# Performance work log

Hardware: AMD Instinct MI355X
Metric: run time of the kernel (lower is better)

Reference implementation:

```python
import math
import jax
import jax.numpy as jnp
import numpy as np

B, T, D = 1, 2048, 1024
H, KV, DH = 16, 4, 64
E, TOPK, DFF = 32, 4, 1024
WINDOW = 128
EPS = 1e-5
ROPE_BASE = 150000.0
ROPE_SCALE = 32.0


def setup_inputs() -> dict:
    key = jax.random.key(0)
    ks = jax.random.split(key, 12)
    s = 0.02  # init scale for stability
    return {
        "x": jax.random.normal(ks[0], (B, T, D), jnp.float32),
        "attn_norm_w": 1.0 + 0.02 * jax.random.normal(ks[1], (D,), jnp.float32),
        "ffn_norm_w": 1.0 + 0.02 * jax.random.normal(ks[2], (D,), jnp.float32),
        "qkv_w": s * jax.random.normal(ks[3], (D, H * DH + 2 * KV * DH), jnp.float32),
        "qkv_b": s * jax.random.normal(ks[4], (H * DH + 2 * KV * DH,), jnp.float32),
        "proj_w": s * jax.random.normal(ks[5], (H * DH, D), jnp.float32),
        "proj_b": s * jax.random.normal(ks[6], (D,), jnp.float32),
        "attn_sink": 0.5 * jax.random.normal(ks[7], (H,), jnp.float32),
        "gate_w": s * jax.random.normal(ks[8], (D, E), jnp.float32),
        "gate_b": s * jax.random.normal(ks[9], (E,), jnp.float32),
        "W_up": s * jax.random.normal(ks[10], (E, D, 2 * DFF), jnp.float32),
        "W_down": s * jax.random.normal(ks[11], (E, DFF, D), jnp.float32),
    }


def _rmsnorm(x, w):
    rms = jax.lax.rsqrt(jnp.mean(x * x, axis=-1, keepdims=True) + EPS)
    return w * (x * rms)


def _apply_rope(x, sin, cos):
    # x: [B, h, T, dh]; sin/cos: [T, dh//2] -> interleaved rotation
    x1, x2 = x[..., ::2], x[..., 1::2]
    out = jnp.stack([x1 * cos - x2 * sin, x1 * sin + x2 * cos], axis=-1)
    return out.reshape(x.shape)


def reference(x, attn_norm_w, ffn_norm_w, qkv_w, qkv_b, proj_w, proj_b,
              attn_sink, gate_w, gate_b, W_up, W_down):
    Bx, Tx, Dx = x.shape
    # ---- attention branch ----
    h = _rmsnorm(x, attn_norm_w)
    qkv = h @ qkv_w + qkv_b
    q = qkv[..., : H * DH].reshape(Bx, Tx, H, DH).transpose(0, 2, 1, 3)
    k = qkv[..., H * DH : H * DH + KV * DH].reshape(Bx, Tx, KV, DH).transpose(0, 2, 1, 3)
    v = qkv[..., H * DH + KV * DH :].reshape(Bx, Tx, KV, DH).transpose(0, 2, 1, 3)
    # RoPE angles: pos/scale * base^{-2i/dh}
    pos = jnp.arange(Tx, dtype=jnp.float32) / ROPE_SCALE
    inv_freq = 1.0 / (ROPE_BASE ** (jnp.arange(0, DH, 2, dtype=jnp.float32) / DH))
    freqs = pos[:, None] * inv_freq[None, :]  # [T, DH//2]
    sin, cos = jnp.sin(freqs), jnp.cos(freqs)
    q = _apply_rope(q, sin, cos)
    k = _apply_rope(k, sin, cos)
    rep = H // KV
    k = jnp.repeat(k, rep, axis=1)
    v = jnp.repeat(v, rep, axis=1)
    logits = jnp.einsum('bhqd,bhkd->bhqk', q, k) / math.sqrt(DH)
    i = jnp.arange(Tx)[:, None]
    j = jnp.arange(Tx)[None, :]
    mask = (j > i) | (i - j > WINDOW)  # sliding-window causal
    logits = jnp.where(mask, -jnp.inf, logits)
    lse = jax.nn.logsumexp(logits, axis=-1, keepdims=True)  # [B,H,T,1]
    denom_log = jnp.logaddexp(lse, attn_sink.reshape(1, H, 1, 1))
    attn = jnp.exp(logits - denom_log)  # rows sum to < 1 due to sink
    y = jnp.einsum('bhqk,bhkd->bhqd', attn, v)
    y = y.transpose(0, 2, 1, 3).reshape(Bx, Tx, H * DH)
    x = x + (y @ proj_w + proj_b)
    # ---- token-choice MoE branch ----
    h2 = _rmsnorm(x, ffn_norm_w).reshape(Bx * Tx, Dx)
    glogits = h2 @ gate_w + gate_b  # [N, E]
    topv, topi = jax.lax.top_k(glogits, TOPK)
    gw = jax.nn.softmax(topv, axis=-1)  # [N, TOPK]
    N = Bx * Tx
    combine = jnp.zeros((N, E), x.dtype).at[jnp.arange(N)[:, None], topi].add(gw)
    def body(acc, we):
        wu, wd, ce = we  # [D,2DFF], [DFF,D], [N]
        ug = h2 @ wu
        u, g = ug[:, :DFF], ug[:, DFF:]
        return acc + ce[:, None] * ((jax.nn.silu(g) * u) @ wd), None
    y2, _ = jax.lax.scan(body, jnp.zeros_like(h2), (W_up, W_down, combine.T))
    return x + y2.reshape(Bx, Tx, Dx)
```

## Files before the change

### kernel.cpp

```cpp
#include <hip/hip_runtime.h>
#include <hip/hip_bf16.h>

#define NEx 32
#define QKVN 1536
#define MAXTILES 96

typedef __attribute__((ext_vector_type(4))) float f32x4_t;
typedef __attribute__((ext_vector_type(8))) __bf16 bf16x8_t;

__device__ __forceinline__ unsigned short f2bfu(float f) {
  union { float f; unsigned int u; } a; a.f = f;
  unsigned int r = a.u + 0x7fffu + ((a.u >> 16) & 1u);
  return (unsigned short)(r >> 16);
}
__device__ __forceinline__ float bf2f(unsigned short u) {
  union { unsigned int u; float f; } a; a.u = ((unsigned int)u) << 16; return a.f;
}
__device__ __forceinline__ uint2 pack4u(unsigned short a, unsigned short b,
                                        unsigned short c, unsigned short d) {
  return make_uint2((unsigned int)a | ((unsigned int)b << 16),
                    (unsigned int)c | ((unsigned int)d << 16));
}
__device__ __forceinline__ void split2(float v, unsigned short& hi, unsigned short& lo) {
  hi = f2bfu(v);
  lo = f2bfu(v - bf2f(hi));
}
typedef const __attribute__((address_space(1))) void* gas_t;
typedef __attribute__((address_space(3))) void* las_t;
__device__ __forceinline__ void gl16(const void* g, void* l) {
  __builtin_amdgcn_global_load_lds((gas_t)g, (las_t)l, 16, 0, 0);
}

template<int SPLIT>
__global__ __launch_bounds__(256) void k_wT(const float* __restrict__ in,
    unsigned short* __restrict__ outh, unsigned short* __restrict__ outl, int N) {
  __shared__ float T[64][68];
  int k0 = blockIdx.x * 64, n0 = blockIdx.y * 64, e = blockIdx.z;
  const float* src = in + (size_t)e * 1024 * N;
  int t = threadIdx.x;
  int rk = t >> 2, c4 = (t & 3) * 4;
#pragma unroll
  for (int j = 0; j < 4; ++j) {
    int col = c4 + j * 16;
    f32x4_t v = *(const f32x4_t*)(src + (size_t)(k0 + rk) * N + n0 + col);
    *(f32x4_t*)&T[rk][col] = v;
  }
  __syncthreads();
  int nn = t >> 2, kc0 = (t & 3) * 16;
  size_t orow = ((size_t)e * N + n0 + nn) * 1024 + k0;
#pragma unroll
  for (int j = 0; j < 2; ++j) {
    int kc = kc0 + j * 8;
    unsigned short hi[8], lo[8];
#pragma unroll
    for (int q = 0; q < 8; ++q) split2(T[kc + q][nn], hi[q], lo[q]);
    uint2 a = pack4u(hi[0], hi[1], hi[2], hi[3]);
    uint2 b = pack4u(hi[4], hi[5], hi[6], hi[7]);
    *(uint4*)(outh + orow + kc) = make_uint4(a.x, a.y, b.x, b.y);
    if (SPLIT) {
      uint2 c = pack4u(lo[0], lo[1], lo[2], lo[3]);
      uint2 d = pack4u(lo[4], lo[5], lo[6], lo[7]);
      *(uint4*)(outl + orow + kc) = make_uint4(c.x, c.y, d.x, d.y);
    }
  }
}

__global__ __launch_bounds__(256) void k_rmsnorm_s(const float* __restrict__ x,
    const float* __restrict__ w, unsigned short* __restrict__ ph, unsigned short* __restrict__ pl) {
  int row = blockIdx.x, tid = threadIdx.x;
  f32x4_t v = *(const f32x4_t*)(x + (size_t)row * 1024 + tid * 4);
  float ss = v.x * v.x + v.y * v.y + v.z * v.z + v.w * v.w;
#pragma unroll
  for (int o = 32; o > 0; o >>= 1) ss += __shfl_xor(ss, o);
  __shared__ float red[4];
  if ((tid & 63) == 0) red[tid >> 6] = ss;
  __syncthreads();
  float sc = rsqrtf((red[0] + red[1] + red[2] + red[3]) * (1.f / 1024.f) + 1e-5f);
  const float* wr = w + tid * 4;
  ushort4 h4, l4;
  split2(v.x * sc * wr[0], h4.x, l4.x);
  split2(v.y * sc * wr[1], h4.y, l4.y);
  split2(v.z * sc * wr[2], h4.z, l4.z);
  split2(v.w * sc * wr[3], h4.w, l4.w);
  *(ushort4*)(ph + (size_t)row * 1024 + tid * 4) = h4;
  *(ushort4*)(pl + (size_t)row * 1024 + tid * 4) = l4;
}

__global__ __launch_bounds__(256) void k_rmsnorm_f(const float* __restrict__ x,
    const float* __restrict__ w, float* __restrict__ outf, unsigned short* __restrict__ outb,
    float* __restrict__ y2) {
  int row = blockIdx.x, tid = threadIdx.x;
  f32x4_t v = *(const f32x4_t*)(x + (size_t)row * 1024 + tid * 4);
  *(f32x4_t*)(y2 + (size_t)row * 1024 + tid * 4) = (f32x4_t){0.f, 0.f, 0.f, 0.f};
  float ss = v.x * v.x + v.y * v.y + v.z * v.z + v.w * v.w;
#pragma unroll
  for (int o = 32; o > 0; o >>= 1) ss += __shfl_xor(ss, o);
  __shared__ float red[4];
  if ((tid & 63) == 0) red[tid >> 6] = ss;
  __syncthreads();
  float sc = rsqrtf((red[0] + red[1] + red[2] + red[3]) * (1.f / 1024.f) + 1e-5f);
  const float* wr = w + tid * 4;
  f32x4_t o4;
  o4.x = v.x * sc * wr[0]; o4.y = v.y * sc * wr[1];
  o4.z = v.z * sc * wr[2]; o4.w = v.w * sc * wr[3];
  *(f32x4_t*)(outf + (size_t)row * 1024 + tid * 4) = o4;
  ushort4 b4;
  b4.x = f2bfu(o4.x); b4.y = f2bfu(o4.y); b4.z = f2bfu(o4.z); b4.w = f2bfu(o4.w);
  *(ushort4*)(outb + (size_t)row * 1024 + tid * 4) = b4;
}

template<int RES>
__global__ __launch_bounds__(256) void k_gemm_s(
    const unsigned short* __restrict__ Ahg, const unsigned short* __restrict__ Alg,
    const unsigned short* __restrict__ BhT, const unsigned short* __restrict__ BlT,
    const float* __restrict__ bias, const float* __restrict__ res,
    float* __restrict__ C, int N) {
  __shared__ unsigned short Ah[64 * 32], Al[64 * 32], Bh[128 * 32], Bl[128 * 32];
  int tid = threadIdx.x, lane = tid & 63, w = tid >> 6;
  int m0 = blockIdx.y * 64, n0 = blockIdx.x * 128;
  int wm = (w >> 1) * 32, wn = (w & 1) * 64;
  int rl = lane >> 2, koff = (lane & 3) * 8;
  const unsigned short* agh = Ahg + (size_t)(m0 + w * 16 + rl) * 1024 + koff;
  const unsigned short* agl = Alg + (size_t)(m0 + w * 16 + rl) * 1024 + koff;
  const unsigned short* bgh0 = BhT + (size_t)(n0 + (w * 2 + 0) * 16 + rl) * 1024 + koff;
  const unsigned short* bgh1 = BhT + (size_t)(n0 + (w * 2 + 1) * 16 + rl) * 1024 + koff;
  const unsigned short* bgl0 = BlT + (size_t)(n0 + (w * 2 + 0) * 16 + rl) * 1024 + koff;
  const unsigned short* bgl1 = BlT + (size_t)(n0 + (w * 2 + 1) * 16 + rl) * 1024 + koff;
  f32x4_t acc[2][4];
#pragma unroll
  for (int i = 0; i < 2; ++i)
#pragma unroll
    for (int j = 0; j < 4; ++j) acc[i][j] = (f32x4_t){0.f, 0.f, 0.f, 0.f};
  int fr = lane & 15, fc = (lane >> 4) * 8;
  for (int k0 = 0; k0 < 1024; k0 += 32) {
    gl16(agh + k0, (char*)Ah + w * 1024);
    gl16(agl + k0, (char*)Al + w * 1024);
    gl16(bgh0 + k0, (char*)Bh + (w * 2 + 0) * 1024);
    gl16(bgh1 + k0, (char*)Bh + (w * 2 + 1) * 1024);
    gl16(bgl0 + k0, (char*)Bl + (w * 2 + 0) * 1024);
    gl16(bgl1 + k0, (char*)Bl + (w * 2 + 1) * 1024);
    __syncthreads();
    bf16x8_t fah[2], fal[2], fbh[4], fbl[4];
#pragma unroll
    for (int mi = 0; mi < 2; ++mi) {
      fah[mi] = *(const bf16x8_t*)(Ah + (wm + mi * 16 + fr) * 32 + fc);
      fal[mi] = *(const bf16x8_t*)(Al + (wm + mi * 16 + fr) * 32 + fc);
    }
#pragma unroll
    for (int nj = 0; nj < 4; ++nj) {
      fbh[nj] = *(const bf16x8_t*)(Bh + (wn + nj * 16 + fr) * 32 + fc);
      fbl[nj] = *(const bf16x8_t*)(Bl + (wn + nj * 16 + fr) * 32 + fc);
    }
#pragma unroll
    for (int mi = 0; mi < 2; ++mi)
#pragma unroll
      for (int nj = 0; nj < 4; ++nj) {
        acc[mi][nj] = __builtin_amdgcn_mfma_f32_16x16x32_bf16(fah[mi], fbh[nj], acc[mi][nj], 0, 0, 0);
        acc[mi][nj] = __builtin_amdgcn_mfma_f32_16x16x32_bf16(fah[mi], fbl[nj], acc[mi][nj], 0, 0, 0);
        acc[mi][nj] = __builtin_amdgcn_mfma_f32_16x16x32_bf16(fal[mi], fbh[nj], acc[mi][nj], 0, 0, 0);
      }
    __syncthreads();
  }
  int frow = (lane >> 4) * 4;
#pragma unroll
  for (int mi = 0; mi < 2; ++mi)
#pragma unroll
    for (int nj = 0; nj < 4; ++nj) {
      int col = n0 + wn + nj * 16 + fr;
      float bv = bias[col];
#pragma unroll
      for (int r = 0; r < 4; ++r) {
        int row = m0 + wm + mi * 16 + frow + r;
        float v = acc[mi][nj][r] + bv;
        if (RES) v += res[(size_t)row * N + col];
        C[(size_t)row * N + col] = v;
      }
    }
}

__global__ __launch_bounds__(256) void k_rope(float* __restrict__ qkv) {
  int idx = blockIdx.x * 256 + threadIdx.x;
  int i = idx & 31;
  int r5 = idx >> 5;
  int hd = r5 % 20, t = r5 / 20;
  int col = (hd < 16) ? hd * 64 : 1024 + (hd - 16) * 64;
  float* p = qkv + (size_t)t * QKVN + col + 2 * i;
  float2 v = *(float2*)p;
  float invf = exp2f(-(float)i * (17.194602975157967f / 32.f));
  float ang = ((float)t * (1.f / 32.f)) * invf;
  float s, c;
  sincosf(ang, &s, &c);
  float2 o; o.x = v.x * c - v.y * s; o.y = v.x * s + v.y * c;
  *(float2*)p = o;
}

__global__ __launch_bounds__(256) void k_attn(const float* __restrict__ qkv,
    const float* __restrict__ sink, unsigned short* __restrict__ yh,
    unsigned short* __restrict__ yl) {
  __shared__ float Kl[72 * 65];
  __shared__ float Vl[72 * 64];
  __shared__ float ql[16][64];
  __shared__ float pl[4][128];
  int i0 = blockIdx.x * 16, hh = blockIdx.y;
  int g = hh >> 2;
  int jb = i0 - 128; if (jb < 0) jb = 0;
  int nk = i0 + 16 - jb;
  int tid = threadIdx.x, wid = tid >> 6, lane = tid & 63;
  {
    int r = tid >> 4, d4 = (tid & 15) * 4;
    *(f32x4_t*)&ql[r][d4] = *(const f32x4_t*)(qkv + (size_t)(i0 + r) * QKVN + hh * 64 + d4);
  }
  float sk = sink[hh];
  float m_[4], s_[4], y_[4];
#pragma unroll
  for (int qq = 0; qq < 4; ++qq) { m_[qq] = sk; s_[qq] = 0.f; y_[qq] = 0.f; }
  int nch = (nk + 71) / 72;
  int cbase = 0;
  for (int ch = 0; ch < nch; ++ch) {
    int csz = nk - cbase; if (csz > 72) csz = 72;
    __syncthreads();
    for (int id = tid; id < csz * 16; id += 256) {
      int c = id >> 4, d4 = (id & 15) * 4;
      const float* kp = qkv + (size_t)(jb + cbase + c) * QKVN + 1024 + g * 64 + d4;
      *(f32x4_t*)&Kl[c * 65 + d4] = *(const f32x4_t*)kp;
      *(f32x4_t*)&Vl[c * 64 + d4] = *(const f32x4_t*)(kp + 256);
    }
    __syncthreads();
#pragma unroll
    for (int qq = 0; qq < 4; ++qq) {
      int qr = wid * 4 + qq;
      int cm = i0 + qr - jb;
      int s1 = lane + 64;
      int r1 = (s1 < csz) ? s1 : (csz - 1);
      const float* k0p = Kl + lane * 65;
      const float* k1p = Kl + r1 * 65;
      float a0 = 0.f, a1 = 0.f;
#pragma unroll 4
      for (int d = 0; d < 64; ++d) {
        float qd = ql[qr][d];
        a0 += qd * k0p[d];
        a1 += qd * k1p[d];
      }
      int c0 = cbase + lane, c1 = cbase + s1;
      bool ok0 = (lane < csz) && (c0 <= cm) && (c0 >= cm - 128);
      bool ok1 = (s1 < csz) && (c1 <= cm) && (c1 >= cm - 128);
      float l0 = ok0 ? a0 * 0.125f : -1e30f;
      float l1 = ok1 ? a1 * 0.125f : -1e30f;
      float mc = fmaxf(l0, l1);
#pragma unroll
      for (int o = 32; o > 0; o >>= 1) mc = fmaxf(mc, __shfl_xor(mc, o));
      float mo = m_[qq];
      float mn = fmaxf(mo, mc);
      float fac = __expf(mo - mn);
      float p0 = __expf(l0 - mn), p1 = __expf(l1 - mn);
      float ps = p0 + p1;
#pragma unroll
      for (int o = 32; o > 0; o >>= 1) ps += __shfl_xor(ps, o);
      m_[qq] = mn;
      s_[qq] = s_[qq] * fac + ps;
      pl[wid][lane] = p0;
      pl[wid][s1] = p1;
      __syncthreads();
      float y = y_[qq] * fac;
      for (int s = 0; s < csz; ++s) y += pl[wid][s] * Vl[s * 64 + lane];
      y_[qq] = y;
      __syncthreads();
    }
    cbase += csz;
  }
#pragma unroll
  for (int qq = 0; qq < 4; ++qq) {
    float inv = 1.f / (s_[qq] + __expf(sk - m_[qq]));
    int i = i0 + wid * 4 + qq;
    unsigned short hi, lo;
    split2(y_[qq] * inv, hi, lo);
    yh[(size_t)i * 1024 + hh * 64 + lane] = hi;
    yl[(size_t)i * 1024 + hh * 64 + lane] = lo;
  }
}

__global__ __launch_bounds__(64) void k_gate(const float* __restrict__ h2f,
    const float* __restrict__ gw, const float* __restrict__ gb,
    int* __restrict__ texp, float* __restrict__ twt) {
  int t = blockIdx.x, l = threadIdx.x;
  int e = l & 31, half = l >> 5;
  const float* hr = h2f + (size_t)t * 1024 + half * 512;
  const float* wp = gw + (size_t)half * 512 * 32 + e;
  float s = 0;
  for (int d = 0; d < 512; ++d) s += hr[d] * wp[(size_t)d * 32];
  s += __shfl_xor(s, 32);
  __shared__ float gl[32];
  if (l < 32) gl[l] = s + gb[e];
  __syncthreads();
  if (l == 0) {
    int bi[4]; float bv[4];
    for (int j = 0; j < 4; ++j) {
      int mi_ = 0; float mv = gl[0];
      for (int q = 1; q < 32; ++q) if (gl[q] > mv) { mv = gl[q]; mi_ = q; }
      bi[j] = mi_; bv[j] = mv; gl[mi_] = -1e30f;
    }
    float mx = bv[0], sum = 0, wv[4];
    for (int j = 0; j < 4; ++j) { wv[j] = __expf(bv[j] - mx); sum += wv[j]; }
    float inv = 1.f / sum;
    for (int j = 0; j < 4; ++j) { texp[t * 4 + j] = bi[j]; twt[t * 4 + j] = wv[j] * inv; }
  }
}

__global__ __launch_bounds__(256) void k_moe_count(const int* __restrict__ texp, int* __restrict__ cnt) {
  int e = blockIdx.x, tid = threadIdx.x;
  int c = 0;
  for (int i = tid; i < 8192; i += 256) c += (texp[i] == e);
#pragma unroll
  for (int o = 32; o > 0; o >>= 1) c += __shfl_xor(c, o);
  __shared__ int red[4];
  if ((tid & 63) == 0) red[tid >> 6] = c;
  __syncthreads();
  if (tid == 0) cnt[e] = red[0] + red[1] + red[2] + red[3];
}

__global__ void k_moe_off(const int* __restrict__ cnt, int* __restrict__ off,
                          int* __restrict__ tiles) {
  if (threadIdx.x == 0) {
    int s = 0, t = 0;
    for (int e = 0; e < NEx; ++e) {
      off[e] = s;
      int nt = (cnt[e] + 127) >> 7;
      for (int j = 0; j < nt; ++j) tiles[t++] = e | (j << 8);
      s += cnt[e];
    }
    for (; t < MAXTILES; ++t) tiles[t] = -1;
  }
}

__global__ __launch_bounds__(256) void k_moe_assign(const int* __restrict__ texp,
    const float* __restrict__ twt, const int* __restrict__ off,
    int* __restrict__ slot_token, float* __restrict__ slot_wt) {
  int e = blockIdx.x, tid = threadIdx.x;
  int b0 = tid * 32;
  int c = 0;
  for (int i = 0; i < 32; ++i) c += (texp[b0 + i] == e);
  __shared__ int pre[256];
  pre[tid] = c;
  __syncthreads();
  for (int d = 1; d < 256; d <<= 1) {
    int v = (tid >= d) ? pre[tid - d] : 0;
    __syncthreads();
    pre[tid] += v;
    __syncthreads();
  }
  int run = off[e] + pre[tid] - c;
  for (int i = 0; i < 32; ++i) {
    int idx = b0 + i;
    if (texp[idx] == e) {
      slot_token[run] = idx >> 2;
      slot_wt[run] = twt[idx];
      ++run;
    }
  }
}

__global__ __launch_bounds__(256) void k_moe_up(const unsigned short* __restrict__ h2b,
    const unsigned short* __restrict__ WupT, const int* __restrict__ cnt,
    const int* __restrict__ off, const int* __restrict__ tiles,
    const int* __restrict__ slot_token, unsigned short* __restrict__ act) {
  int code = tiles[blockIdx.y];
  if (code < 0) return;
  int e = code & 255;
  int m0 = (code >> 8) << 7;
  int ne = cnt[e];
  int n0 = blockIdx.x * 64;
  int base = off[e];
  __shared__ unsigned short Asm[128 * 32];
  __shared__ unsigned short Bsm[128 * 32];
  int tid = threadIdx.x, lane = tid & 63, w = tid >> 6;
  int rl = lane >> 2, koff = (lane & 3) * 8;
  const unsigned short* ag[2];
  const unsigned short* bg[2];
#pragma unroll
  for (int i = 0; i < 2; ++i) {
    int row = (w * 2 + i) * 16 + rl;
    int tok = (m0 + row < ne) ? slot_token[base + m0 + row] : 0;
    ag[i] = h2b + (size_t)tok * 1024 + koff;
    int grow = (row < 64) ? (n0 + row) : (1024 + n0 + row - 64);
    bg[i] = WupT + (size_t)e * 2048 * 1024 + (size_t)grow * 1024 + koff;
  }
  f32x4_t acc[2][8];
#pragma unroll
  for (int i = 0; i < 2; ++i)
#pragma unroll
    for (int j = 0; j < 8; ++j) acc[i][j] = (f32x4_t){0.f, 0.f, 0.f, 0.f};
  int fr = lane & 15, fc = (lane >> 4) * 8;
  for (int k0 = 0; k0 < 1024; k0 += 32) {
    gl16(ag[0] + k0, (char*)Asm + (w * 2 + 0) * 1024);
    gl16(ag[1] + k0, (char*)Asm + (w * 2 + 1) * 1024);
    gl16(bg[0] + k0, (char*)Bsm + (w * 2 + 0) * 1024);
    gl16(bg[1] + k0, (char*)Bsm + (w * 2 + 1) * 1024);
    __syncthreads();
    bf16x8_t af[2], bfr[8];
#pragma unroll
    for (int mi = 0; mi < 2; ++mi)
      af[mi] = *(const bf16x8_t*)(Asm + (w * 32 + mi * 16 + fr) * 32 + fc);
#pragma unroll
    for (int nj = 0; nj < 8; ++nj)
      bfr[nj] = *(const bf16x8_t*)(Bsm + (nj * 16 + fr) * 32 + fc);
#pragma unroll
    for (int mi = 0; mi < 2; ++mi)
#pragma unroll
      for (int nj = 0; nj < 8; ++nj)
        acc[mi][nj] = __builtin_amdgcn_mfma_f32_16x16x32_bf16(af[mi], bfr[nj], acc[mi][nj], 0, 0, 0);
    __syncthreads();
  }
  int frow = (lane >> 4) * 4;
#pragma unroll
  for (int mi = 0; mi < 2; ++mi)
#pragma unroll
    for (int r = 0; r < 4; ++r) {
      int row = m0 + w * 32 + mi * 16 + frow + r;
      if (row < ne) {
#pragma unroll
        for (int nj = 0; nj < 4; ++nj) {
          float u = acc[mi][nj][r];
          float gg = acc[mi][nj + 4][r];
          float sig = 1.f / (1.f + __expf(-gg));
          act[(size_t)(base + row) * 1024 + n0 + nj * 16 + fr] = f2bfu(u * gg * sig);
        }
      }
    }
}

__global__ __launch_bounds__(256) void k_moe_down(const unsigned short* __restrict__ act,
    const unsigned short* __restrict__ WdnT, const int* __restrict__ cnt,
    const int* __restrict__ off, const int* __restrict__ tiles,
    const int* __restrict__ slot_token, const float* __restrict__ slot_wt,
    float* __restrict__ y2) {
  int code = tiles[blockIdx.y];
  if (code < 0) return;
  int e = code & 255;
  int m0 = (code >> 8) << 7;
  int ne = cnt[e];
  int n0 = blockIdx.x * 128;
  int base = off[e];
  __shared__ unsigned short Asm[128 * 32];
  __shared__ unsigned short Bsm[128 * 32];
  int tid = threadIdx.x, lane = tid & 63, w = tid >> 6;
  int wm = (w >> 1) * 64, wn = (w & 1) * 64;
  int rl = lane >> 2, koff = (lane & 3) * 8;
  const unsigned short* ag[2];
  const unsigned short* bg[2];
#pragma unroll
  for (int i = 0; i < 2; ++i) {
    int row = (w * 2 + i) * 16 + rl;
    ag[i] = act + (size_t)(base + m0 + row) * 1024 + koff;
    bg[i] = WdnT + (size_t)e * 1024 * 1024 + (size_t)(n0 + row) * 1024 + koff;
  }
  f32x4_t acc[4][4];
#pragma unroll
  for (int i = 0; i < 4; ++i)
#pragma unroll
    for (int j = 0; j < 4; ++j) acc[i][j] = (f32x4_t){0.f, 0.f, 0.f, 0.f};
  int fr = lane & 15, fc = (lane >> 4) * 8;
  for (int k0 = 0; k0 < 1024; k0 += 32) {
    gl16(ag[0] + k0, (char*)Asm + (w * 2 + 0) * 1024);
    gl16(ag[1] + k0, (char*)Asm + (w * 2 + 1) * 1024);
    gl16(bg[0] + k0, (char*)Bsm + (w * 2 + 0) * 1024);
    gl16(bg[1] + k0, (char*)Bsm + (w * 2 + 1) * 1024);
    __syncthreads();
    bf16x8_t af[4], bfr[4];
#pragma unroll
    for (int mi = 0; mi < 4; ++mi)
      af[mi] = *(const bf16x8_t*)(Asm + (wm + mi * 16 + fr) * 32 + fc);
#pragma unroll
    for (int nj = 0; nj < 4; ++nj)
      bfr[nj] = *(const bf16x8_t*)(Bsm + (wn + nj * 16 + fr) * 32 + fc);
#pragma unroll
    for (int mi = 0; mi < 4; ++mi)
#pragma unroll
      for (int nj = 0; nj < 4; ++nj)
        acc[mi][nj] = __builtin_amdgcn_mfma_f32_16x16x32_bf16(af[mi], bfr[nj], acc[mi][nj], 0, 0, 0);
    __syncthreads();
  }
  int frow = (lane >> 4) * 4;
#pragma unroll
  for (int mi = 0; mi < 4; ++mi)
#pragma unroll
    for (int r = 0; r < 4; ++r) {
      int row = m0 + wm + mi * 16 + frow + r;
      if (row < ne) {
        int slot = base + row;
        int token = slot_token[slot];
        float wt = slot_wt[slot];
#pragma unroll
        for (int nj = 0; nj < 4; ++nj) {
          int col = n0 + wn + nj * 16 + fr;
          atomicAdd(&y2[(size_t)token * 1024 + col], wt * acc[mi][nj][r]);
        }
      }
    }
}

__global__ __launch_bounds__(256) void k_final(const float* __restrict__ x1,
    const float* __restrict__ y2, float* __restrict__ out) {
  int idx = blockIdx.x * 256 + threadIdx.x;
  f32x4_t a = *(const f32x4_t*)(x1 + (size_t)idx * 4);
  f32x4_t b = *(const f32x4_t*)(y2 + (size_t)idx * 4);
  a = a + b;
  *(f32x4_t*)(out + (size_t)idx * 4) = a;
}

extern "C" void kernel_launch(void* const* d_in, const int* in_sizes, int n_in,
                              void* d_out, int out_size, void* d_ws, size_t ws_size,
                              hipStream_t stream) {
  const float* x           = (const float*)d_in[0];
  const float* attn_norm_w = (const float*)d_in[1];
  const float* ffn_norm_w  = (const float*)d_in[2];
  const float* qkv_w       = (const float*)d_in[3];
  const float* qkv_b       = (const float*)d_in[4];
  const float* proj_w      = (const float*)d_in[5];
  const float* proj_b      = (const float*)d_in[6];
  const float* attn_sink   = (const float*)d_in[7];
  const float* gate_w      = (const float*)d_in[8];
  const float* gate_b      = (const float*)d_in[9];
  const float* W_up        = (const float*)d_in[10];
  const float* W_down      = (const float*)d_in[11];
  float* out = (float*)d_out;

  char* ws = (char*)d_ws;
  size_t o = 0;
  auto alloc = [&](size_t bytes) -> void* {
    void* p = ws + o;
    o = (o + bytes + 255) & ~(size_t)255;
    return p;
  };
  unsigned short* WT      = (unsigned short*)alloc((size_t)32 * 2048 * 1024 * 2);
  unsigned short* qkvThi  = (unsigned short*)alloc((size_t)1536 * 1024 * 2);
  unsigned short* qkvTlo  = (unsigned short*)alloc((size_t)1536 * 1024 * 2);
  unsigned short* projThi = (unsigned short*)alloc((size_t)1024 * 1024 * 2);
  unsigned short* projTlo = (unsigned short*)alloc((size_t)1024 * 1024 * 2);
  unsigned short* pAhi    = (unsigned short*)alloc((size_t)2048 * 1024 * 2);
  unsigned short* pAlo    = (unsigned short*)alloc((size_t)2048 * 1024 * 2);
  float* qkv              = (float*)alloc((size_t)2048 * 1536 * 4);
  float* x1               = (float*)alloc((size_t)2048 * 1024 * 4);
  unsigned short* act     = (unsigned short*)alloc((size_t)(8192 + 128) * 1024 * 2);
  float* y2               = (float*)alloc((size_t)2048 * 1024 * 4);
  int* texp               = (int*)alloc(8192 * 4);
  float* twt              = (float*)alloc(8192 * 4);
  int* cnt                = (int*)alloc(256);
  int* offs               = (int*)alloc(256);
  int* tiles              = (int*)alloc(MAXTILES * 4);
  int* slot_token         = (int*)alloc(8192 * 4);
  float* slot_wt          = (float*)alloc(8192 * 4);
  float* h2f              = qkv;
  unsigned short* h2b     = (unsigned short*)(qkv + (size_t)2048 * 1024);

  k_wT<1><<<dim3(16, 24, 1), 256, 0, stream>>>(qkv_w, qkvThi, qkvTlo, 1536);
  k_wT<1><<<dim3(16, 16, 1), 256, 0, stream>>>(proj_w, projThi, projTlo, 1024);
  k_wT<0><<<dim3(16, 32, 32), 256, 0, stream>>>(W_up, WT, nullptr, 2048);

  k_rmsnorm_s<<<2048, 256, 0, stream>>>(x, attn_norm_w, pAhi, pAlo);
  k_gemm_s<0><<<dim3(12, 32), 256, 0, stream>>>(pAhi, pAlo, qkvThi, qkvTlo, qkv_b, nullptr, qkv, 1536);
  k_rope<<<5120, 256, 0, stream>>>(qkv);
  k_attn<<<dim3(128, 16), 256, 0, stream>>>(qkv, attn_sink, pAhi, pAlo);
  k_gemm_s<1><<<dim3(8, 32), 256, 0, stream>>>(pAhi, pAlo, projThi, projTlo, proj_b, x, x1, 1024);
  k_rmsnorm_f<<<2048, 256, 0, stream>>>(x1, ffn_norm_w, h2f, h2b, y2);
  k_gate<<<2048, 64, 0, stream>>>(h2f, gate_w, gate_b, texp, twt);
  k_moe_count<<<32, 256, 0, stream>>>(texp, cnt);
  k_moe_off<<<1, 64, 0, stream>>>(cnt, offs, tiles);
  k_moe_assign<<<32, 256, 0, stream>>>(texp, twt, offs, slot_token, slot_wt);
  k_moe_up<<<dim3(16, MAXTILES), 256, 0, stream>>>(h2b, WT, cnt, offs, tiles, slot_token, act);
  k_wT<0><<<dim3(16, 16, 32), 256, 0, stream>>>(W_down, WT, nullptr, 1024);
  k_moe_down<<<dim3(8, MAXTILES), 256, 0, stream>>>(act, WT, cnt, offs, tiles, slot_token, slot_wt, y2);
  k_final<<<2048, 256, 0, stream>>>(x1, y2, out);
}
```

Before: 475.9 us.

## Restructure attention to batch four queries per warp and fuse residual into output

```diff
diff --git a/kernel.cpp b/kernel.cpp
--- a/kernel.cpp
+++ b/kernel.cpp
@@ -88,10 +88,10 @@
 
 __global__ __launch_bounds__(256) void k_rmsnorm_f(const float* __restrict__ x,
     const float* __restrict__ w, float* __restrict__ outf, unsigned short* __restrict__ outb,
-    float* __restrict__ y2) {
+    float* __restrict__ out) {
   int row = blockIdx.x, tid = threadIdx.x;
   f32x4_t v = *(const f32x4_t*)(x + (size_t)row * 1024 + tid * 4);
-  *(f32x4_t*)(y2 + (size_t)row * 1024 + tid * 4) = (f32x4_t){0.f, 0.f, 0.f, 0.f};
+  *(f32x4_t*)(out + (size_t)row * 1024 + tid * 4) = v;
   float ss = v.x * v.x + v.y * v.y + v.z * v.z + v.w * v.w;
 #pragma unroll
   for (int o = 32; o > 0; o >>= 1) ss += __shfl_xor(ss, o);
@@ -200,7 +200,7 @@
   __shared__ float Kl[72 * 65];
   __shared__ float Vl[72 * 64];
   __shared__ float ql[16][64];
-  __shared__ float pl[4][128];
+  __shared__ float pl[4][4][128];
   int i0 = blockIdx.x * 16, hh = blockIdx.y;
   int g = hh >> 2;
   int jb = i0 - 128; if (jb < 0) jb = 0;
@@ -216,6 +216,7 @@
   for (int qq = 0; qq < 4; ++qq) { m_[qq] = sk; s_[qq] = 0.f; y_[qq] = 0.f; }
   int nch = (nk + 71) / 72;
   int cbase = 0;
+  int qb = wid * 4;
   for (int ch = 0; ch < nch; ++ch) {
     int csz = nk - cbase; if (csz > 72) csz = 72;
     __syncthreads();
@@ -226,26 +227,30 @@
       *(f32x4_t*)&Vl[c * 64 + d4] = *(const f32x4_t*)(kp + 256);
     }
     __syncthreads();
+    int s1 = lane + 64;
+    int r1 = (s1 < csz) ? s1 : (csz - 1);
+    const float* k0p = Kl + lane * 65;
+    const float* k1p = Kl + r1 * 65;
+    float a0[4] = {0.f, 0.f, 0.f, 0.f}, a1[4] = {0.f, 0.f, 0.f, 0.f};
+#pragma unroll 4
+    for (int d = 0; d < 64; ++d) {
+      float k0 = k0p[d], k1 = k1p[d];
+#pragma unroll
+      for (int qq = 0; qq < 4; ++qq) {
+        float qd = ql[qb + qq][d];
+        a0[qq] += qd * k0;
+        a1[qq] += qd * k1;
+      }
+    }
+    int c0 = cbase + lane, c1 = cbase + s1;
+    float fac_[4];
 #pragma unroll
     for (int qq = 0; qq < 4; ++qq) {
-      int qr = wid * 4 + qq;
-      int cm = i0 + qr - jb;
-      int s1 = lane + 64;
-      int r1 = (s1 < csz) ? s1 : (csz - 1);
-      const float* k0p = Kl + lane * 65;
-      const float* k1p = Kl + r1 * 65;
-      float a0 = 0.f, a1 = 0.f;
-#pragma unroll 4
-      for (int d = 0; d < 64; ++d) {
-        float qd = ql[qr][d];
-        a0 += qd * k0p[d];
-        a1 += qd * k1p[d];
-      }
-      int c0 = cbase + lane, c1 = cbase + s1;
+      int cm = i0 + qb + qq - jb;
       bool ok0 = (lane < csz) && (c0 <= cm) && (c0 >= cm - 128);
       bool ok1 = (s1 < csz) && (c1 <= cm) && (c1 >= cm - 128);
-      float l0 = ok0 ? a0 * 0.125f : -1e30f;
-      float l1 = ok1 ? a1 * 0.125f : -1e30f;
+      float l0 = ok0 ? a0[qq] * 0.125f : -1e30f;
+      float l1 = ok1 ? a1[qq] * 0.125f : -1e30f;
       float mc = fmaxf(l0, l1);
 #pragma unroll
       for (int o = 32; o > 0; o >>= 1) mc = fmaxf(mc, __shfl_xor(mc, o));
@@ -258,20 +263,25 @@
       for (int o = 32; o > 0; o >>= 1) ps += __shfl_xor(ps, o);
       m_[qq] = mn;
       s_[qq] = s_[qq] * fac + ps;
-      pl[wid][lane] = p0;
-      pl[wid][s1] = p1;
-      __syncthreads();
-      float y = y_[qq] * fac;
-      for (int s = 0; s < csz; ++s) y += pl[wid][s] * Vl[s * 64 + lane];
-      y_[qq] = y;
-      __syncthreads();
+      pl[wid][qq][lane] = p0;
+      pl[wid][qq][s1] = p1;
+      fac_[qq] = fac;
+    }
+#pragma unroll
+    for (int qq = 0; qq < 4; ++qq) y_[qq] *= fac_[qq];
+    for (int s = 0; s < csz; ++s) {
+      float v = Vl[s * 64 + lane];
+      y_[0] += pl[wid][0][s] * v;
+      y_[1] += pl[wid][1][s] * v;
+      y_[2] += pl[wid][2][s] * v;
+      y_[3] += pl[wid][3][s] * v;
     }
     cbase += csz;
   }
 #pragma unroll
   for (int qq = 0; qq < 4; ++qq) {
     float inv = 1.f / (s_[qq] + __expf(sk - m_[qq]));
-    int i = i0 + wid * 4 + qq;
+    int i = i0 + qb + qq;
     unsigned short hi, lo;
     split2(y_[qq] * inv, hi, lo);
     yh[(size_t)i * 1024 + hh * 64 + lane] = hi;
@@ -432,7 +442,7 @@
     const unsigned short* __restrict__ WdnT, const int* __restrict__ cnt,
     const int* __restrict__ off, const int* __restrict__ tiles,
     const int* __restrict__ slot_token, const float* __restrict__ slot_wt,
-    float* __restrict__ y2) {
+    float* __restrict__ out) {
   int code = tiles[blockIdx.y];
   if (code < 0) return;
   int e = code & 255;
@@ -492,19 +502,10 @@
 #pragma unroll
         for (int nj = 0; nj < 4; ++nj) {
           int col = n0 + wn + nj * 16 + fr;
-          atomicAdd(&y2[(size_t)token * 1024 + col], wt * acc[mi][nj][r]);
+          atomicAdd(&out[(size_t)token * 1024 + col], wt * acc[mi][nj][r]);
         }
       }
     }
-}
-
-__global__ __launch_bounds__(256) void k_final(const float* __restrict__ x1,
-    const float* __restrict__ y2, float* __restrict__ out) {
-  int idx = blockIdx.x * 256 + threadIdx.x;
-  f32x4_t a = *(const f32x4_t*)(x1 + (size_t)idx * 4);
-  f32x4_t b = *(const f32x4_t*)(y2 + (size_t)idx * 4);
-  a = a + b;
-  *(f32x4_t*)(out + (size_t)idx * 4) = a;
 }
 
 extern "C" void kernel_launch(void* const* d_in, const int* in_sizes, int n_in,
@@ -541,7 +542,6 @@
   float* qkv              = (float*)alloc((size_t)2048 * 1536 * 4);
   float* x1               = (float*)alloc((size_t)2048 * 1024 * 4);
   unsigned short* act     = (unsigned short*)alloc((size_t)(8192 + 128) * 1024 * 2);
-  float* y2               = (float*)alloc((size_t)2048 * 1024 * 4);
   int* texp               = (int*)alloc(8192 * 4);
   float* twt              = (float*)alloc(8192 * 4);
   int* cnt                = (int*)alloc(256);
@@ -561,13 +561,12 @@
   k_rope<<<5120, 256, 0, stream>>>(qkv);
   k_attn<<<dim3(128, 16), 256, 0, stream>>>(qkv, attn_sink, pAhi, pAlo);
   k_gemm_s<1><<<dim3(8, 32), 256, 0, stream>>>(pAhi, pAlo, projThi, projTlo, proj_b, x, x1, 1024);
-  k_rmsnorm_f<<<2048, 256, 0, stream>>>(x1, ffn_norm_w, h2f, h2b, y2);
+  k_rmsnorm_f<<<2048, 256, 0, stream>>>(x1, ffn_norm_w, h2f, h2b, out);
   k_gate<<<2048, 64, 0, stream>>>(h2f, gate_w, gate_b, texp, twt);
   k_moe_count<<<32, 256, 0, stream>>>(texp, cnt);
   k_moe_off<<<1, 64, 0, stream>>>(cnt, offs, tiles);
   k_moe_assign<<<32, 256, 0, stream>>>(texp, twt, offs, slot_token, slot_wt);
   k_moe_up<<<dim3(16, MAXTILES), 256, 0, stream>>>(h2b, WT, cnt, offs, tiles, slot_token, act);
   k_wT<0><<<dim3(16, 16, 32), 256, 0, stream>>>(W_down, WT, nullptr, 1024);
-  k_moe_down<<<dim3(8, MAXTILES), 256, 0, stream>>>(act, WT, cnt, offs, tiles, slot_token, slot_wt, y2);
-  k_final<<<2048, 256, 0, stream>>>(x1, y2, out);
-}
+  k_moe_down<<<dim3(8, MAXTILES), 256, 0, stream>>>(act, WT, cnt, offs, tiles, slot_token, slot_wt, out);
+}
```

After: 433.5 us. 1.1x faster.
